# Kernel optimization log

Measured on AMD Instinct MI355X. Metric: run time of the kernel, lower is better.

## Reference

```python
import jax, jax.numpy as jnp
import numpy as np

THRESHOLD = 0.5
NEG_POS = 3
ALPHA = 0.5
EPS = 1e-6


def cxcy2xy(b):
    return jnp.concatenate([b[:, :2] - b[:, 2:] / 2, b[:, :2] + b[:, 2:] / 2], axis=1)


def xy2cxcy(b):
    return jnp.concatenate([(b[:, 2:] + b[:, :2]) / 2, b[:, 2:] - b[:, :2]], axis=1)


def encode_boxes(b, d):
    return jnp.concatenate([(b[:, :2] - d[:, :2]) / (d[:, 2:] / 10 + EPS),
                            jnp.log(b[:, 2:] / d[:, 2:] + EPS) * 5], axis=1)


def find_iou(a, b):
    # a: [O,4] xy, b: [N,4] xy -> [O,N]
    lt = jnp.maximum(a[:, None, :2], b[None, :, :2])
    rb = jnp.minimum(a[:, None, 2:], b[None, :, 2:])
    wh = jnp.clip(rb - lt, 0.0)
    inter = wh[..., 0] * wh[..., 1]
    area_a = (a[:, 2] - a[:, 0]) * (a[:, 3] - a[:, 1])
    area_b = (b[:, 2] - b[:, 0]) * (b[:, 3] - b[:, 1])
    return inter / (area_a[:, None] + area_b[None, :] - inter)


def _match(boxes_i, labels_i, def_xy, default_boxes):
    # boxes_i: [O,4] xy, labels_i: [O], def_xy/default_boxes: [N,4]
    n_obj = boxes_i.shape[0]
    overlap = find_iou(boxes_i, def_xy)            # [O, N]
    overlap_defbox = overlap.max(axis=0)           # [N]
    object_defbox = overlap.argmax(axis=0)         # [N]
    defbox_object = overlap.argmax(axis=1)         # [O]
    object_defbox = object_defbox.at[defbox_object].set(jnp.arange(n_obj))
    overlap_defbox = overlap_defbox.at[defbox_object].set(1.0)
    label = labels_i[object_defbox]
    label = jnp.where(overlap_defbox < THRESHOLD, 0, label)
    t_loc = encode_boxes(xy2cxcy(boxes_i[object_defbox]), default_boxes)
    return t_loc, label


def reference(locs_pred, cls_pred, boxes, labels, default_boxes):
    B, N, C = cls_pred.shape
    def_xy = cxcy2xy(default_boxes)
    t_locs, t_classes = jax.vmap(_match, in_axes=(0, 0, None, None))(
        boxes, labels, def_xy, default_boxes)      # [B,N,4], [B,N]

    pos = t_classes != 0                            # [B,N]
    n_pos = pos.sum(axis=1)                         # [B]
    n_pos_total = n_pos.sum().astype(jnp.float32)

    # SmoothL1 (beta=1), mean over positive-box coordinate elements
    d = jnp.abs(locs_pred - t_locs)
    sl1 = jnp.where(d < 1.0, 0.5 * d * d, d - 0.5)
    loc_loss = jnp.sum(sl1 * pos[..., None].astype(sl1.dtype)) / (n_pos_total * 4.0)

    # per-anchor cross entropy
    logp = jax.nn.log_softmax(cls_pred, axis=-1)
    all_conf = -jnp.take_along_axis(logp, t_classes[..., None], axis=-1)[..., 0]  # [B,N]

    pos_conf = jnp.sum(jnp.where(pos, all_conf, 0.0))
    neg_conf = jnp.where(pos, 0.0, all_conf)
    neg_sorted = -jnp.sort(-neg_conf, axis=1)       # descending
    hard = jnp.arange(N)[None, :] < (NEG_POS * n_pos)[:, None]
    hard_sum = jnp.sum(jnp.where(hard, neg_sorted, 0.0))

    conf_loss = (hard_sum + pos_conf) / n_pos_total
    return ALPHA * loc_loss + conf_loss


def setup_inputs() -> dict:
    key = jax.random.key(0)
    k1, k2, k3, k4, k5, k6, k7 = jax.random.split(key, 7)
    B, N, C, O = 32, 24564, 81, 16
    locs_pred = jax.random.normal(k1, (B, N, 4), dtype=jnp.float32)
    cls_pred = jax.random.normal(k2, (B, N, C), dtype=jnp.float32)
    # ground-truth boxes: valid xy boxes inside [0,1]
    cxy = jax.random.uniform(k3, (B, O, 2), minval=0.2, maxval=0.8)
    wh = jax.random.uniform(k4, (B, O, 2), minval=0.05, maxval=0.3)
    boxes = jnp.concatenate([cxy - wh / 2, cxy + wh / 2], axis=-1).astype(jnp.float32)
    labels = jax.random.randint(k5, (B, O), 1, C)
    dcxy = jax.random.uniform(k6, (N, 2), minval=0.05, maxval=0.95)
    dwh = jax.random.uniform(k7, (N, 2), minval=0.05, maxval=0.4)
    default_boxes = jnp.concatenate([dcxy, dwh], axis=-1).astype(jnp.float32)
    return {"locs_pred": locs_pred, "cls_pred": cls_pred, "boxes": boxes,
            "labels": labels, "default_boxes": default_boxes}
```

## Files before the change

### kernel.cpp

```cpp
#include <hip/hip_runtime.h>
#include <math.h>

#define THRESH    0.5f
#define NEG_POSK  3
#define EPSf      1e-6f
#define CCLS      81
#define TILEA     64
#define CHUNKS    16
#define TPB       16

__device__ __forceinline__ float iou_xy(float ax0, float ay0, float ax1, float ay1,
                                        float bx0, float by0, float bx1, float by1) {
    float lx = fmaxf(ax0, bx0), ly = fmaxf(ay0, by0);
    float rx = fminf(ax1, bx1), ry = fminf(ay1, by1);
    float w = fmaxf(rx - lx, 0.f), h = fmaxf(ry - ly, 0.f);
    float inter = w * h;
    float aa = (ax1 - ax0) * (ay1 - ay0);
    float ab = (bx1 - bx0) * (by1 - by0);
    return inter / (aa + ab - inter);
}

__device__ __forceinline__ void gload16(const void* g, void* l) {
    __builtin_amdgcn_global_load_lds(
        (const __attribute__((address_space(1))) void*)g,
        (__attribute__((address_space(3))) void*)l, 16, 0, 0);
}

__global__ __launch_bounds__(256) void k_obj_part(const float* __restrict__ boxes,
                                                  const float* __restrict__ dboxes,
                                                  float* __restrict__ part_iou,
                                                  int* __restrict__ part_idx,
                                                  int N, int O) {
    int bo = blockIdx.x;
    int c  = blockIdx.y;
    const float* bb = boxes + (size_t)bo * 4;
    float ax0 = bb[0], ay0 = bb[1], ax1 = bb[2], ay1 = bb[3];
    int chunk = (N + CHUNKS - 1) / CHUNKS;
    int n0 = c * chunk;
    int n1 = min(n0 + chunk, N);
    float best = -1.f; int bi = 0x7FFFFFFF;
    for (int n = n0 + threadIdx.x; n < n1; n += 256) {
        float4 d = ((const float4*)dboxes)[n];
        float dx0 = d.x - d.z * 0.5f, dy0 = d.y - d.w * 0.5f;
        float dx1 = d.x + d.z * 0.5f, dy1 = d.y + d.w * 0.5f;
        float iou = iou_xy(ax0, ay0, ax1, ay1, dx0, dy0, dx1, dy1);
        if (iou > best) { best = iou; bi = n; }
    }
    #pragma unroll
    for (int dd = 1; dd < 64; dd <<= 1) {
        float v2 = __shfl_xor(best, dd); int i2 = __shfl_xor(bi, dd);
        if (v2 > best || (v2 == best && i2 < bi)) { best = v2; bi = i2; }
    }
    __shared__ float sv[4]; __shared__ int si[4];
    int w = threadIdx.x >> 6;
    if ((threadIdx.x & 63) == 0) { sv[w] = best; si[w] = bi; }
    __syncthreads();
    if (threadIdx.x == 0) {
        #pragma unroll
        for (int i = 1; i < 4; ++i)
            if (sv[i] > best || (sv[i] == best && si[i] < bi)) { best = sv[i]; bi = si[i]; }
        part_iou[(size_t)bo * CHUNKS + c] = best;
        part_idx[(size_t)bo * CHUNKS + c] = bi;
    }
}

__global__ void k_obj_reduce(const float* __restrict__ part_iou,
                             const int* __restrict__ part_idx,
                             int* __restrict__ defbox_object, int BO) {
    int bo = blockIdx.x * blockDim.x + threadIdx.x;
    if (bo >= BO) return;
    float best = -1.f; int bi = 0x7FFFFFFF;
    #pragma unroll
    for (int c = 0; c < CHUNKS; ++c) {
        float v = part_iou[(size_t)bo * CHUNKS + c];
        int  i = part_idx[(size_t)bo * CHUNKS + c];
        if (v > best || (v == best && i < bi)) { best = v; bi = i; }
    }
    defbox_object[bo] = bi;
}

template<int OT>
__global__ __launch_bounds__(256)
void k_conf(const float* __restrict__ locs_pred,
            const float* __restrict__ cls,
            const float* __restrict__ boxes,
            const int* __restrict__ labels,
            const float* __restrict__ dboxes,
            const int* __restrict__ dbo_g,
            float* __restrict__ vneg,
            int* __restrict__ n_pos,
            float* __restrict__ loc_sum,
            float* __restrict__ pos_conf,
            int N, int O_rt, int bpb, int tilesPerBatch) {
    const int O = OT ? OT : O_rt;
    __shared__ __align__(16) float sm[2][TILEA * CCLS];
    __shared__ float sbb[64];
    __shared__ int slab[16], sdbo[16];
    __shared__ float swl[4], swp[4];
    __shared__ int swc[4];
    const int tid = threadIdx.x;
    const int b  = blockIdx.x / bpb;
    const int t0 = (blockIdx.x % bpb) * TPB;
    const int tEnd = min(t0 + TPB, tilesPerBatch);

    if (tid < O * 4) sbb[tid] = boxes[(size_t)b * O * 4 + tid];
    else if (tid < O * 5) slab[tid - O * 4] = labels[(size_t)b * O + tid - O * 4];
    else if (tid < O * 6) sdbo[tid - O * 5] = dbo_g[(size_t)b * O + tid - O * 5];

    const int lane = tid & 63, w = tid >> 6;
    const int j = lane & 15, q = lane >> 4;

    auto stage = [&](int buf, int t) {
        int a0 = t * TILEA;
        int valid = min(TILEA, N - a0);
        const float4* g4 = (const float4*)(cls + ((size_t)b * N + a0) * CCLS);
        float4* s4 = (float4*)sm[buf];
        if (valid == TILEA) {
            #pragma unroll
            for (int k2 = 0; k2 < 5; ++k2) {
                int i4 = w * 64 + k2 * 256;
                gload16(g4 + i4 + lane, s4 + i4);
            }
            if (tid < 16) gload16(g4 + 1280 + tid, s4 + 1280);
        } else {
            int len = valid * CCLS;
            const float* g = (const float*)g4;
            for (int i = tid; i < len; i += 256) sm[buf][i] = g[i];
        }
    };

    float pc = 0.f, ls = 0.f; int cnt = 0;

    auto phase2 = [&](int buf, int t) {
        int a0 = t * TILEA;
        int valid = min(TILEA, N - a0);
        int a = w * 16 + j;
        const float* row = &sm[buf][a * CCLS];
        float s = 0.f;
        bool act = a < valid;
        if (act) {
            int c0 = q * 20;
            #pragma unroll
            for (int i = 0; i < 20; ++i) s += __expf(row[c0 + i]);
            if (q == 3) s += __expf(row[80]);
        }
        s += __shfl_xor(s, 16);
        s += __shfl_xor(s, 32);
        if (act && q == 0) {
            int n = a0 + a;
            float4 d = ((const float4*)dboxes)[n];
            float dx0 = d.x - d.z * 0.5f, dy0 = d.y - d.w * 0.5f;
            float dx1 = d.x + d.z * 0.5f, dy1 = d.y + d.w * 0.5f;
            float best = -1.f; int sel = 0;
            #pragma unroll
            for (int o = 0; o < O; ++o) {
                float iou = iou_xy(sbb[o*4], sbb[o*4+1], sbb[o*4+2], sbb[o*4+3],
                                   dx0, dy0, dx1, dy1);
                if (iou > best) { best = iou; sel = o; }
            }
            bool forced = false;
            #pragma unroll
            for (int o = 0; o < O; ++o)
                if (sdbo[o] == n) { sel = o; forced = true; }
            float iou_eff = forced ? 1.0f : best;
            int lbl = (iou_eff < THRESH) ? 0 : slab[sel];
            float conf = __logf(s) - row[lbl];
            bool pos = (lbl != 0);
            size_t idx = (size_t)b * N + n;
            vneg[idx] = pos ? 0.f : conf;
            if (pos) {
                pc += conf; cnt++;
                float bx0 = sbb[sel*4], by0 = sbb[sel*4+1];
                float bx1 = sbb[sel*4+2], by1 = sbb[sel*4+3];
                float bcx = (bx0 + bx1) * 0.5f, bcy = (by0 + by1) * 0.5f;
                float bw = bx1 - bx0, bh = by1 - by0;
                float t0f = (bcx - d.x) / (d.z / 10.0f + EPSf);
                float t1f = (bcy - d.y) / (d.w / 10.0f + EPSf);
                float t2f = __logf(bw / d.z + EPSf) * 5.0f;
                float t3f = __logf(bh / d.w + EPSf) * 5.0f;
                float4 p = ((const float4*)locs_pred)[idx];
                float dd;
                dd = fabsf(p.x - t0f); ls += (dd < 1.f) ? 0.5f*dd*dd : dd - 0.5f;
                dd = fabsf(p.y - t1f); ls += (dd < 1.f) ? 0.5f*dd*dd : dd - 0.5f;
                dd = fabsf(p.z - t2f); ls += (dd < 1.f) ? 0.5f*dd*dd : dd - 0.5f;
                dd = fabsf(p.w - t3f); ls += (dd < 1.f) ? 0.5f*dd*dd : dd - 0.5f;
            }
        }
    };

    stage(0, t0);
    __syncthreads();
    int cur = 0;
    for (int t = t0; t < tEnd; ++t) {
        if (t + 1 < tEnd) stage(cur ^ 1, t + 1);
        phase2(cur, t);
        __syncthreads();
        cur ^= 1;
    }

    #pragma unroll
    for (int dd = 1; dd < 64; dd <<= 1) {
        pc  += __shfl_xor(pc, dd);
        ls  += __shfl_xor(ls, dd);
        cnt += __shfl_xor(cnt, dd);
    }
    if (lane == 0) { swp[w] = pc; swl[w] = ls; swc[w] = cnt; }
    __syncthreads();
    if (tid == 0) {
        float P = swp[0] + swp[1] + swp[2] + swp[3];
        float L = swl[0] + swl[1] + swl[2] + swl[3];
        int   C = swc[0] + swc[1] + swc[2] + swc[3];
        if (C) {
            atomicAdd(&n_pos[b], C);
            atomicAdd(loc_sum, L);
            atomicAdd(pos_conf, P);
        }
    }
}

__device__ void wave_select(const int* hist, int nbins, int k, int* out_bin, int* out_k) {
    int lane = threadIdx.x & 63;
    int cum = 0;
    for (int c = nbins / 64 - 1; c >= 0; --c) {
        int val = hist[c * 64 + lane];
        int s = val;
        for (int d = 1; d < 64; d <<= 1) {
            int t = __shfl_down(s, d);
            if (lane + d < 64) s += t;
        }
        int total = __shfl(s, 0);
        if (cum + total >= k) {
            unsigned long long mask = __ballot(cum + s >= k);
            int bl = 63 - __builtin_clzll(mask);
            int sB = __shfl(s, bl);
            int vB = __shfl(val, bl);
            if (lane == 0) {
                *out_bin = c * 64 + bl;
                *out_k = k - (cum + sB - vB);
            }
            return;
        }
        cum += total;
    }
    if (lane == 0) { *out_bin = 0; *out_k = 1; }
}

__global__ __launch_bounds__(1024) void k_select(const float* __restrict__ vneg,
                                                 const int* __restrict__ n_pos,
                                                 float* __restrict__ hard_sum,
                                                 int B, int N) {
    int b = blockIdx.x;
    const float* v = vneg + (size_t)b * N;
    __shared__ int hist[2048];
    __shared__ int bcast_bin, bcast_k;
    __shared__ float swv[16];
    __shared__ int swc[16];
    int np = n_pos[b];
    long long kk = (long long)NEG_POSK * np;
    if (kk > N) kk = N;
    int k = (int)kk;
    if (k <= 0) return;
    int tid = threadIdx.x;

    for (int i = tid; i < 2048; i += 1024) hist[i] = 0;
    __syncthreads();
    for (int n = tid; n < N; n += 1024) {
        unsigned u = __float_as_uint(v[n]);
        atomicAdd(&hist[u >> 20], 1);
    }
    __syncthreads();
    if (tid < 64) wave_select(hist, 2048, k, &bcast_bin, &bcast_k);
    __syncthreads();
    int B1 = bcast_bin, k2 = bcast_k;

    for (int i = tid; i < 2048; i += 1024) hist[i] = 0;
    __syncthreads();
    for (int n = tid; n < N; n += 1024) {
        unsigned u = __float_as_uint(v[n]);
        if ((int)(u >> 20) == B1) atomicAdd(&hist[(u >> 9) & 0x7FF], 1);
    }
    __syncthreads();
    if (tid < 64) wave_select(hist, 2048, k2, &bcast_bin, &bcast_k);
    __syncthreads();
    int B2 = bcast_bin, k3 = bcast_k;
    unsigned pre = ((unsigned)B1 << 11) | (unsigned)B2;

    for (int i = tid; i < 512; i += 1024) hist[i] = 0;
    __syncthreads();
    for (int n = tid; n < N; n += 1024) {
        unsigned u = __float_as_uint(v[n]);
        if ((u >> 9) == pre) atomicAdd(&hist[u & 0x1FF], 1);
    }
    __syncthreads();
    if (tid < 64) wave_select(hist, 512, k3, &bcast_bin, &bcast_k);
    __syncthreads();
    unsigned tau_bits = (pre << 9) | (unsigned)bcast_bin;
    float tau = __uint_as_float(tau_bits);

    float ssum = 0.f; int scnt = 0;
    for (int n = tid; n < N; n += 1024) {
        float x = v[n];
        if (x > tau) { ssum += x; scnt++; }
    }
    for (int d = 1; d < 64; d <<= 1) {
        ssum += __shfl_xor(ssum, d);
        scnt += __shfl_xor(scnt, d);
    }
    int w = tid >> 6;
    if ((tid & 63) == 0) { swv[w] = ssum; swc[w] = scnt; }
    __syncthreads();
    if (tid == 0) {
        float S = 0.f; int Ct = 0;
        for (int i = 0; i < 16; ++i) { S += swv[i]; Ct += swc[i]; }
        float hb = S + (float)(k - Ct) * tau;
        atomicAdd(hard_sum, hb);
    }
}

__global__ void k_final(const int* __restrict__ n_pos,
                        const float* __restrict__ loc_sum,
                        const float* __restrict__ pos_conf,
                        const float* __restrict__ hard_sum,
                        float* __restrict__ out, int B) {
    if (threadIdx.x == 0 && blockIdx.x == 0) {
        int tot = 0;
        for (int b = 0; b < B; ++b) tot += n_pos[b];
        float np = (float)tot;
        float loc = *loc_sum / (np * 4.0f);
        float conf = (*hard_sum + *pos_conf) / np;
        out[0] = 0.5f * loc + conf;
    }
}

extern "C" void kernel_launch(void* const* d_in, const int* in_sizes, int n_in,
                              void* d_out, int out_size, void* d_ws, size_t ws_size,
                              hipStream_t stream) {
    const float* locs_pred = (const float*)d_in[0];
    const float* cls_pred  = (const float*)d_in[1];
    const float* boxes     = (const float*)d_in[2];
    const int*   labels    = (const int*)d_in[3];
    const float* dboxes    = (const float*)d_in[4];

    int N = in_sizes[4] / 4;
    int B = in_sizes[0] / (4 * N);
    int O = in_sizes[3] / B;
    int BO = B * O;

    size_t BN = (size_t)B * N;
    char* ws = (char*)d_ws;
    int*   n_pos    = (int*)ws;
    float* loc_sum  = (float*)(ws + 128);
    float* pos_conf = (float*)(ws + 132);
    float* hard_sum = (float*)(ws + 136);
    float* vneg     = (float*)(ws + 256);
    int*   defbox_object = (int*)(ws + 256 + BN * 4);
    float* part_iou = (float*)(ws + 256 + BN * 4 + (size_t)BO * 4);
    int*   part_idx = (int*)(part_iou + (size_t)BO * CHUNKS);

    hipMemsetAsync(ws, 0, 256, stream);

    dim3 gop(BO, CHUNKS);
    k_obj_part<<<gop, 256, 0, stream>>>(boxes, dboxes, part_iou, part_idx, N, O);
    k_obj_reduce<<<(BO + 255) / 256, 256, 0, stream>>>(part_iou, part_idx,
                                                       defbox_object, BO);
    int tilesPerBatch = (N + TILEA - 1) / TILEA;
    int bpb = (tilesPerBatch + TPB - 1) / TPB;
    dim3 gc(B * bpb);
    if (O == 16)
        k_conf<16><<<gc, 256, 0, stream>>>(locs_pred, cls_pred, boxes, labels, dboxes,
                                           defbox_object, vneg, n_pos, loc_sum,
                                           pos_conf, N, O, bpb, tilesPerBatch);
    else
        k_conf<0><<<gc, 256, 0, stream>>>(locs_pred, cls_pred, boxes, labels, dboxes,
                                          defbox_object, vneg, n_pos, loc_sum,
                                          pos_conf, N, O, bpb, tilesPerBatch);
    k_select<<<B, 1024, 0, stream>>>(vneg, n_pos, hard_sum, B, N);
    k_final<<<1, 1, 0, stream>>>(n_pos, loc_sum, pos_conf, hard_sum, (float*)d_out, B);
}
```

Baseline: 147.9 us.

## Split hard-negative radix select across multi-block histogram kernels and shrink conf tiles

```diff
diff --git a/kernel.cpp b/kernel.cpp
--- a/kernel.cpp
+++ b/kernel.cpp
@@ -5,9 +5,10 @@
 #define NEG_POSK  3
 #define EPSf      1e-6f
 #define CCLS      81
-#define TILEA     64
+#define TILEA     32
 #define CHUNKS    16
-#define TPB       16
+#define TPB       14
+#define NCH2      8
 
 __device__ __forceinline__ float iou_xy(float ax0, float ay0, float ax1, float ay1,
                                         float bx0, float by0, float bx1, float by1) {
@@ -108,7 +109,7 @@
     else if (tid < O * 6) sdbo[tid - O * 5] = dbo_g[(size_t)b * O + tid - O * 5];
 
     const int lane = tid & 63, w = tid >> 6;
-    const int j = lane & 15, q = lane >> 4;
+    const int al = lane >> 3, q = lane & 7;
 
     auto stage = [&](int buf, int t) {
         int a0 = t * TILEA;
@@ -116,12 +117,10 @@
         const float4* g4 = (const float4*)(cls + ((size_t)b * N + a0) * CCLS);
         float4* s4 = (float4*)sm[buf];
         if (valid == TILEA) {
-            #pragma unroll
-            for (int k2 = 0; k2 < 5; ++k2) {
-                int i4 = w * 64 + k2 * 256;
-                gload16(g4 + i4 + lane, s4 + i4);
-            }
-            if (tid < 16) gload16(g4 + 1280 + tid, s4 + 1280);
+            int base = w * 162;
+            gload16(g4 + base + lane, s4 + base);
+            gload16(g4 + base + 64 + lane, s4 + base + 64);
+            if (lane < 34) gload16(g4 + base + 128 + lane, s4 + base + 128);
         } else {
             int len = valid * CCLS;
             const float* g = (const float*)g4;
@@ -134,18 +133,19 @@
     auto phase2 = [&](int buf, int t) {
         int a0 = t * TILEA;
         int valid = min(TILEA, N - a0);
-        int a = w * 16 + j;
+        int a = w * 8 + al;
         const float* row = &sm[buf][a * CCLS];
         float s = 0.f;
         bool act = a < valid;
         if (act) {
-            int c0 = q * 20;
+            int c0 = q * 10;
             #pragma unroll
-            for (int i = 0; i < 20; ++i) s += __expf(row[c0 + i]);
-            if (q == 3) s += __expf(row[80]);
-        }
-        s += __shfl_xor(s, 16);
-        s += __shfl_xor(s, 32);
+            for (int i = 0; i < 10; ++i) s += __expf(row[c0 + i]);
+            if (q == 7) s += __expf(row[80]);
+        }
+        s += __shfl_xor(s, 1);
+        s += __shfl_xor(s, 2);
+        s += __shfl_xor(s, 4);
         if (act && q == 0) {
             int n = a0 + a;
             float4 d = ((const float4*)dboxes)[n];
@@ -188,7 +188,7 @@
         }
     };
 
-    stage(0, t0);
+    if (t0 < tEnd) stage(0, t0);
     __syncthreads();
     int cur = 0;
     for (int t = t0; t < tEnd; ++t) {
@@ -218,117 +218,198 @@
     }
 }
 
-__device__ void wave_select(const int* hist, int nbins, int k, int* out_bin, int* out_k) {
+template<int WORDS>
+__device__ __forceinline__ int2 wave_sel(const int* __restrict__ hist, int k) {
     int lane = threadIdx.x & 63;
-    int cum = 0;
-    for (int c = nbins / 64 - 1; c >= 0; --c) {
-        int val = hist[c * 64 + lane];
+    int vals[WORDS];
+    #pragma unroll
+    for (int j = 0; j < WORDS; ++j) vals[j] = hist[j * 64 + lane];
+    int cum = 0, bin = 0, krem = 1; bool found = false;
+    #pragma unroll
+    for (int j = WORDS - 1; j >= 0; --j) {
+        int val = vals[j];
         int s = val;
+        #pragma unroll
         for (int d = 1; d < 64; d <<= 1) {
             int t = __shfl_down(s, d);
             if (lane + d < 64) s += t;
         }
         int total = __shfl(s, 0);
-        if (cum + total >= k) {
+        if (!found && cum + total >= k) {
             unsigned long long mask = __ballot(cum + s >= k);
             int bl = 63 - __builtin_clzll(mask);
             int sB = __shfl(s, bl);
             int vB = __shfl(val, bl);
-            if (lane == 0) {
-                *out_bin = c * 64 + bl;
-                *out_k = k - (cum + sB - vB);
-            }
-            return;
+            bin = j * 64 + bl;
+            krem = k - (cum + sB - vB);
+            found = true;
         }
         cum += total;
     }
-    if (lane == 0) { *out_bin = 0; *out_k = 1; }
-}
-
-__global__ __launch_bounds__(1024) void k_select(const float* __restrict__ vneg,
-                                                 const int* __restrict__ n_pos,
-                                                 float* __restrict__ hard_sum,
-                                                 int B, int N) {
-    int b = blockIdx.x;
-    const float* v = vneg + (size_t)b * N;
-    __shared__ int hist[2048];
-    __shared__ int bcast_bin, bcast_k;
-    __shared__ float swv[16];
-    __shared__ int swc[16];
-    int np = n_pos[b];
-    long long kk = (long long)NEG_POSK * np;
-    if (kk > N) kk = N;
-    int k = (int)kk;
-    if (k <= 0) return;
-    int tid = threadIdx.x;
-
-    for (int i = tid; i < 2048; i += 1024) hist[i] = 0;
-    __syncthreads();
-    for (int n = tid; n < N; n += 1024) {
-        unsigned u = __float_as_uint(v[n]);
-        atomicAdd(&hist[u >> 20], 1);
-    }
-    __syncthreads();
-    if (tid < 64) wave_select(hist, 2048, k, &bcast_bin, &bcast_k);
-    __syncthreads();
-    int B1 = bcast_bin, k2 = bcast_k;
-
-    for (int i = tid; i < 2048; i += 1024) hist[i] = 0;
-    __syncthreads();
-    for (int n = tid; n < N; n += 1024) {
-        unsigned u = __float_as_uint(v[n]);
-        if ((int)(u >> 20) == B1) atomicAdd(&hist[(u >> 9) & 0x7FF], 1);
-    }
-    __syncthreads();
-    if (tid < 64) wave_select(hist, 2048, k2, &bcast_bin, &bcast_k);
-    __syncthreads();
-    int B2 = bcast_bin, k3 = bcast_k;
-    unsigned pre = ((unsigned)B1 << 11) | (unsigned)B2;
-
-    for (int i = tid; i < 512; i += 1024) hist[i] = 0;
-    __syncthreads();
-    for (int n = tid; n < N; n += 1024) {
-        unsigned u = __float_as_uint(v[n]);
-        if ((u >> 9) == pre) atomicAdd(&hist[u & 0x1FF], 1);
-    }
-    __syncthreads();
-    if (tid < 64) wave_select(hist, 512, k3, &bcast_bin, &bcast_k);
-    __syncthreads();
-    unsigned tau_bits = (pre << 9) | (unsigned)bcast_bin;
-    float tau = __uint_as_float(tau_bits);
-
+    return make_int2(bin, krem);
+}
+
+__global__ __launch_bounds__(256) void kh1(const float* __restrict__ vneg,
+                                           int* __restrict__ ghist1, int N) {
+    int b = blockIdx.x, c = blockIdx.y;
+    __shared__ int h[2048];
+    for (int i = threadIdx.x; i < 2048; i += 256) h[i] = 0;
+    __syncthreads();
+    const float4* v4 = (const float4*)(vneg + (size_t)b * N);
+    int nv = N >> 2;
+    int ch = (nv + NCH2 - 1) / NCH2;
+    int i0 = c * ch, i1 = min(i0 + ch, nv);
+    for (int i = i0 + threadIdx.x; i < i1; i += 256) {
+        float4 x = v4[i];
+        atomicAdd(&h[__float_as_uint(x.x) >> 20], 1);
+        atomicAdd(&h[__float_as_uint(x.y) >> 20], 1);
+        atomicAdd(&h[__float_as_uint(x.z) >> 20], 1);
+        atomicAdd(&h[__float_as_uint(x.w) >> 20], 1);
+    }
+    __syncthreads();
+    int* g = ghist1 + b * 2048;
+    for (int i = threadIdx.x; i < 2048; i += 256)
+        if (h[i]) atomicAdd(&g[i], h[i]);
+}
+
+__global__ __launch_bounds__(256) void kh2(const float* __restrict__ vneg,
+                                           const int* __restrict__ n_pos,
+                                           const int* __restrict__ ghist1,
+                                           int* __restrict__ ghist2, int N) {
+    int b = blockIdx.x, c = blockIdx.y;
+    int k = min(NEG_POSK * n_pos[b], N);
+    __shared__ int sB1;
+    __shared__ int h[2048];
+    for (int i = threadIdx.x; i < 2048; i += 256) h[i] = 0;
+    if (threadIdx.x < 64) {
+        int2 r = wave_sel<32>(ghist1 + b * 2048, k);
+        if (threadIdx.x == 0) sB1 = r.x;
+    }
+    __syncthreads();
+    unsigned B1 = (unsigned)sB1;
+    const float4* v4 = (const float4*)(vneg + (size_t)b * N);
+    int nv = N >> 2;
+    int ch = (nv + NCH2 - 1) / NCH2;
+    int i0 = c * ch, i1 = min(i0 + ch, nv);
+    for (int i = i0 + threadIdx.x; i < i1; i += 256) {
+        float4 x = v4[i];
+        unsigned ux = __float_as_uint(x.x), uy = __float_as_uint(x.y);
+        unsigned uz = __float_as_uint(x.z), uw = __float_as_uint(x.w);
+        if ((ux >> 20) == B1) atomicAdd(&h[(ux >> 9) & 0x7FF], 1);
+        if ((uy >> 20) == B1) atomicAdd(&h[(uy >> 9) & 0x7FF], 1);
+        if ((uz >> 20) == B1) atomicAdd(&h[(uz >> 9) & 0x7FF], 1);
+        if ((uw >> 20) == B1) atomicAdd(&h[(uw >> 9) & 0x7FF], 1);
+    }
+    __syncthreads();
+    int* g = ghist2 + b * 2048;
+    for (int i = threadIdx.x; i < 2048; i += 256)
+        if (h[i]) atomicAdd(&g[i], h[i]);
+}
+
+__global__ __launch_bounds__(256) void kh3(const float* __restrict__ vneg,
+                                           const int* __restrict__ n_pos,
+                                           const int* __restrict__ ghist1,
+                                           const int* __restrict__ ghist2,
+                                           int* __restrict__ ghist3, int N) {
+    int b = blockIdx.x, c = blockIdx.y;
+    int k = min(NEG_POSK * n_pos[b], N);
+    __shared__ int sPre;
+    __shared__ int h[512];
+    for (int i = threadIdx.x; i < 512; i += 256) h[i] = 0;
+    if (threadIdx.x < 64) {
+        int2 r1 = wave_sel<32>(ghist1 + b * 2048, k);
+        int2 r2 = wave_sel<32>(ghist2 + b * 2048, r1.y);
+        if (threadIdx.x == 0) sPre = (r1.x << 11) | r2.x;
+    }
+    __syncthreads();
+    unsigned pre = (unsigned)sPre;
+    const float4* v4 = (const float4*)(vneg + (size_t)b * N);
+    int nv = N >> 2;
+    int ch = (nv + NCH2 - 1) / NCH2;
+    int i0 = c * ch, i1 = min(i0 + ch, nv);
+    for (int i = i0 + threadIdx.x; i < i1; i += 256) {
+        float4 x = v4[i];
+        unsigned ux = __float_as_uint(x.x), uy = __float_as_uint(x.y);
+        unsigned uz = __float_as_uint(x.z), uw = __float_as_uint(x.w);
+        if ((ux >> 9) == pre) atomicAdd(&h[ux & 0x1FF], 1);
+        if ((uy >> 9) == pre) atomicAdd(&h[uy & 0x1FF], 1);
+        if ((uz >> 9) == pre) atomicAdd(&h[uz & 0x1FF], 1);
+        if ((uw >> 9) == pre) atomicAdd(&h[uw & 0x1FF], 1);
+    }
+    __syncthreads();
+    int* g = ghist3 + b * 512;
+    for (int i = threadIdx.x; i < 512; i += 256)
+        if (h[i]) atomicAdd(&g[i], h[i]);
+}
+
+__global__ __launch_bounds__(256) void kscan(const float* __restrict__ vneg,
+                                             const int* __restrict__ n_pos,
+                                             const int* __restrict__ ghist1,
+                                             const int* __restrict__ ghist2,
+                                             const int* __restrict__ ghist3,
+                                             float* __restrict__ hard_s,
+                                             int* __restrict__ hard_c,
+                                             float* __restrict__ tau_arr, int N) {
+    int b = blockIdx.x, c = blockIdx.y;
+    int k = min(NEG_POSK * n_pos[b], N);
+    __shared__ float stau;
+    if (threadIdx.x < 64) {
+        int2 r1 = wave_sel<32>(ghist1 + b * 2048, k);
+        int2 r2 = wave_sel<32>(ghist2 + b * 2048, r1.y);
+        int2 r3 = wave_sel<8>(ghist3 + b * 512, r2.y);
+        if (threadIdx.x == 0)
+            stau = __uint_as_float(((unsigned)r1.x << 20) | ((unsigned)r2.x << 9)
+                                   | (unsigned)r3.x);
+    }
+    __syncthreads();
+    float tau = stau;
+    const float4* v4 = (const float4*)(vneg + (size_t)b * N);
+    int nv = N >> 2;
+    int ch = (nv + NCH2 - 1) / NCH2;
+    int i0 = c * ch, i1 = min(i0 + ch, nv);
     float ssum = 0.f; int scnt = 0;
-    for (int n = tid; n < N; n += 1024) {
-        float x = v[n];
-        if (x > tau) { ssum += x; scnt++; }
-    }
+    for (int i = i0 + threadIdx.x; i < i1; i += 256) {
+        float4 x = v4[i];
+        if (x.x > tau) { ssum += x.x; scnt++; }
+        if (x.y > tau) { ssum += x.y; scnt++; }
+        if (x.z > tau) { ssum += x.z; scnt++; }
+        if (x.w > tau) { ssum += x.w; scnt++; }
+    }
+    #pragma unroll
     for (int d = 1; d < 64; d <<= 1) {
         ssum += __shfl_xor(ssum, d);
         scnt += __shfl_xor(scnt, d);
     }
-    int w = tid >> 6;
-    if ((tid & 63) == 0) { swv[w] = ssum; swc[w] = scnt; }
-    __syncthreads();
-    if (tid == 0) {
-        float S = 0.f; int Ct = 0;
-        for (int i = 0; i < 16; ++i) { S += swv[i]; Ct += swc[i]; }
-        float hb = S + (float)(k - Ct) * tau;
-        atomicAdd(hard_sum, hb);
+    __shared__ float swv[4]; __shared__ int swc[4];
+    int w = threadIdx.x >> 6;
+    if ((threadIdx.x & 63) == 0) { swv[w] = ssum; swc[w] = scnt; }
+    __syncthreads();
+    if (threadIdx.x == 0) {
+        float S = swv[0] + swv[1] + swv[2] + swv[3];
+        int Ct = swc[0] + swc[1] + swc[2] + swc[3];
+        if (S != 0.f || Ct != 0) { atomicAdd(&hard_s[b], S); atomicAdd(&hard_c[b], Ct); }
+        if (c == 0) tau_arr[b] = stau;
     }
 }
 
 __global__ void k_final(const int* __restrict__ n_pos,
                         const float* __restrict__ loc_sum,
                         const float* __restrict__ pos_conf,
-                        const float* __restrict__ hard_sum,
-                        float* __restrict__ out, int B) {
+                        const float* __restrict__ hard_s,
+                        const int* __restrict__ hard_c,
+                        const float* __restrict__ tau_arr,
+                        float* __restrict__ out, int B, int N) {
     if (threadIdx.x == 0 && blockIdx.x == 0) {
         int tot = 0;
         for (int b = 0; b < B; ++b) tot += n_pos[b];
         float np = (float)tot;
+        float hard = 0.f;
+        for (int b = 0; b < B; ++b) {
+            int k = min(NEG_POSK * n_pos[b], N);
+            hard += hard_s[b] + (float)(k - hard_c[b]) * tau_arr[b];
+        }
         float loc = *loc_sum / (np * 4.0f);
-        float conf = (*hard_sum + *pos_conf) / np;
-        out[0] = 0.5f * loc + conf;
+        out[0] = 0.5f * loc + (hard + *pos_conf) / np;
     }
 }
 
@@ -351,13 +432,19 @@
     int*   n_pos    = (int*)ws;
     float* loc_sum  = (float*)(ws + 128);
     float* pos_conf = (float*)(ws + 132);
-    float* hard_sum = (float*)(ws + 136);
-    float* vneg     = (float*)(ws + 256);
-    int*   defbox_object = (int*)(ws + 256 + BN * 4);
-    float* part_iou = (float*)(ws + 256 + BN * 4 + (size_t)BO * 4);
+    float* tau_arr  = (float*)(ws + 192);
+    float* hard_s   = (float*)(ws + 320);
+    int*   hard_c   = (int*)(ws + 448);
+    int*   ghist1   = (int*)(ws + 1024);
+    int*   ghist2   = ghist1 + (size_t)B * 2048;
+    int*   ghist3   = ghist2 + (size_t)B * 2048;
+    int*   defbox_object = ghist3 + (size_t)B * 512;
+    float* part_iou = (float*)(defbox_object + BO);
     int*   part_idx = (int*)(part_iou + (size_t)BO * CHUNKS);
-
-    hipMemsetAsync(ws, 0, 256, stream);
+    float* vneg     = (float*)(part_idx + (size_t)BO * CHUNKS);
+
+    size_t zero_bytes = 1024 + ((size_t)B * 2048 * 2 + (size_t)B * 512) * 4;
+    hipMemsetAsync(ws, 0, zero_bytes, stream);
 
     dim3 gop(BO, CHUNKS);
     k_obj_part<<<gop, 256, 0, stream>>>(boxes, dboxes, part_iou, part_idx, N, O);
@@ -374,6 +461,12 @@
         k_conf<0><<<gc, 256, 0, stream>>>(locs_pred, cls_pred, boxes, labels, dboxes,
                                           defbox_object, vneg, n_pos, loc_sum,
                                           pos_conf, N, O, bpb, tilesPerBatch);
-    k_select<<<B, 1024, 0, stream>>>(vneg, n_pos, hard_sum, B, N);
-    k_final<<<1, 1, 0, stream>>>(n_pos, loc_sum, pos_conf, hard_sum, (float*)d_out, B);
-}
+    dim3 gs(B, NCH2);
+    kh1<<<gs, 256, 0, stream>>>(vneg, ghist1, N);
+    kh2<<<gs, 256, 0, stream>>>(vneg, n_pos, ghist1, ghist2, N);
+    kh3<<<gs, 256, 0, stream>>>(vneg, n_pos, ghist1, ghist2, ghist3, N);
+    kscan<<<gs, 256, 0, stream>>>(vneg, n_pos, ghist1, ghist2, ghist3,
+                                  hard_s, hard_c, tau_arr, N);
+    k_final<<<1, 1, 0, stream>>>(n_pos, loc_sum, pos_conf, hard_s, hard_c, tau_arr,
+                                 (float*)d_out, B, N);
+}
```

Result: slower. 213.8 us (+44.6%).

## Triple-buffer class-score staging with explicit vmcnt waits and uniform async loads

Applied to the files above, without the earlier changes.

```diff
diff --git a/kernel.cpp b/kernel.cpp
--- a/kernel.cpp
+++ b/kernel.cpp
@@ -7,7 +7,8 @@
 #define CCLS      81
 #define TILEA     64
 #define CHUNKS    16
-#define TPB       16
+#define TPB       12
+#define NBUF      3
 
 __device__ __forceinline__ float iou_xy(float ax0, float ay0, float ax1, float ay1,
                                         float bx0, float by0, float bx1, float by1) {
@@ -91,9 +92,9 @@
             int* __restrict__ n_pos,
             float* __restrict__ loc_sum,
             float* __restrict__ pos_conf,
-            int N, int O_rt, int bpb, int tilesPerBatch) {
+            int N, int O_rt, int bpb, int tilesPerBatch, long long totalF4) {
     const int O = OT ? OT : O_rt;
-    __shared__ __align__(16) float sm[2][TILEA * CCLS];
+    __shared__ __align__(16) float sm[NBUF][TILEA * CCLS];
     __shared__ float sbb[64];
     __shared__ int slab[16], sdbo[16];
     __shared__ float swl[4], swp[4];
@@ -111,21 +112,18 @@
     const int j = lane & 15, q = lane >> 4;
 
     auto stage = [&](int buf, int t) {
-        int a0 = t * TILEA;
-        int valid = min(TILEA, N - a0);
-        const float4* g4 = (const float4*)(cls + ((size_t)b * N + a0) * CCLS);
+        long long base4 = (((long long)b * N + (long long)t * TILEA) * CCLS) >> 2;
+        const float4* g4 = (const float4*)cls + base4;
         float4* s4 = (float4*)sm[buf];
-        if (valid == TILEA) {
+        long long cap = totalF4 - base4;
+        if (lane < 54) {
             #pragma unroll
-            for (int k2 = 0; k2 < 5; ++k2) {
-                int i4 = w * 64 + k2 * 256;
-                gload16(g4 + i4 + lane, s4 + i4);
+            for (int k2 = 0; k2 < 6; ++k2) {
+                int c = (w * 6 + k2) * 54;
+                long long gi = c + lane;
+                if (gi >= cap) gi = cap - 1;
+                gload16(g4 + gi, s4 + c);
             }
-            if (tid < 16) gload16(g4 + 1280 + tid, s4 + 1280);
-        } else {
-            int len = valid * CCLS;
-            const float* g = (const float*)g4;
-            for (int i = tid; i < len; i += 256) sm[buf][i] = g[i];
         }
     };
 
@@ -136,8 +134,8 @@
         int valid = min(TILEA, N - a0);
         int a = w * 16 + j;
         const float* row = &sm[buf][a * CCLS];
+        bool act = a < valid;
         float s = 0.f;
-        bool act = a < valid;
         if (act) {
             int c0 = q * 20;
             #pragma unroll
@@ -148,7 +146,9 @@
         s += __shfl_xor(s, 32);
         if (act && q == 0) {
             int n = a0 + a;
+            size_t idx = (size_t)b * N + n;
             float4 d = ((const float4*)dboxes)[n];
+            float4 p = ((const float4*)locs_pred)[idx];
             float dx0 = d.x - d.z * 0.5f, dy0 = d.y - d.w * 0.5f;
             float dx1 = d.x + d.z * 0.5f, dy1 = d.y + d.w * 0.5f;
             float best = -1.f; int sel = 0;
@@ -166,7 +166,6 @@
             int lbl = (iou_eff < THRESH) ? 0 : slab[sel];
             float conf = __logf(s) - row[lbl];
             bool pos = (lbl != 0);
-            size_t idx = (size_t)b * N + n;
             vneg[idx] = pos ? 0.f : conf;
             if (pos) {
                 pc += conf; cnt++;
@@ -178,7 +177,6 @@
                 float t1f = (bcy - d.y) / (d.w / 10.0f + EPSf);
                 float t2f = __logf(bw / d.z + EPSf) * 5.0f;
                 float t3f = __logf(bh / d.w + EPSf) * 5.0f;
-                float4 p = ((const float4*)locs_pred)[idx];
                 float dd;
                 dd = fabsf(p.x - t0f); ls += (dd < 1.f) ? 0.5f*dd*dd : dd - 0.5f;
                 dd = fabsf(p.y - t1f); ls += (dd < 1.f) ? 0.5f*dd*dd : dd - 0.5f;
@@ -189,13 +187,17 @@
     };
 
     stage(0, t0);
-    __syncthreads();
-    int cur = 0;
+    stage(1, min(t0 + 1, tEnd - 1));
     for (int t = t0; t < tEnd; ++t) {
-        if (t + 1 < tEnd) stage(cur ^ 1, t + 1);
-        phase2(cur, t);
-        __syncthreads();
-        cur ^= 1;
+        int it = t - t0;
+        if (it == 0)
+            asm volatile("s_waitcnt vmcnt(6) lgkmcnt(0)" ::: "memory");
+        else
+            asm volatile("s_waitcnt vmcnt(9)" ::: "memory");
+        __builtin_amdgcn_s_barrier();
+        __builtin_amdgcn_sched_barrier(0);
+        stage((it + 2) % NBUF, min(t + 2, tEnd - 1));
+        phase2(it % NBUF, t);
     }
 
     #pragma unroll
@@ -365,15 +367,16 @@
                                                        defbox_object, BO);
     int tilesPerBatch = (N + TILEA - 1) / TILEA;
     int bpb = (tilesPerBatch + TPB - 1) / TPB;
+    long long totalF4 = ((long long)B * N * CCLS) >> 2;
     dim3 gc(B * bpb);
     if (O == 16)
         k_conf<16><<<gc, 256, 0, stream>>>(locs_pred, cls_pred, boxes, labels, dboxes,
                                            defbox_object, vneg, n_pos, loc_sum,
-                                           pos_conf, N, O, bpb, tilesPerBatch);
+                                           pos_conf, N, O, bpb, tilesPerBatch, totalF4);
     else
         k_conf<0><<<gc, 256, 0, stream>>>(locs_pred, cls_pred, boxes, labels, dboxes,
                                           defbox_object, vneg, n_pos, loc_sum,
-                                          pos_conf, N, O, bpb, tilesPerBatch);
+                                          pos_conf, N, O, bpb, tilesPerBatch, totalF4);
     k_select<<<B, 1024, 0, stream>>>(vneg, n_pos, hard_sum, B, N);
     k_final<<<1, 1, 0, stream>>>(n_pos, loc_sum, pos_conf, hard_sum, (float*)d_out, B);
 }
```

New measurement: 167.7 us. 13.4% more time.
